# Performance work log

Hardware: AMD Instinct MI355X
Metric: run time of the kernel (lower is better)

Reference implementation:

```python
import jax, jax.numpy as jnp
import numpy as np
import itertools

R_MAX = 0.4
POWER = 0
B, N_ATOMS, K_OPS = 16, 256, 16

# 27 periodic image shifts, same order as itertools.product([0,1,-1], repeat=3)
SHIFTS = jnp.asarray(list(itertools.product([0, 1, -1], repeat=3)), dtype=jnp.float32)  # [27,3]


def _pair_sq_sum(f, r):
    """sum over neighbor pairs (dist<=r) of elementwise (frac_dst-frac_src)**2.

    Equivalent to torch get_neighbors (cdist over 27 shifted copies, radius
    mask, gather) followed by (vec*vec).sum(dim=0), without materializing
    the variable-length edge list. f: [N,3] -> out: [3]."""
    n = f.shape[0]
    # shift-major replication: f_ex[s*n + i] = f[i] + SHIFTS[s], matching
    # torch.cat([frac]*27) + shifts.repeat_interleave(n)
    f_ex = (f[None, :, :] + SHIFTS[:, None, :]).reshape(27 * n, 3)
    d = f_ex[None, :, :] - f[:, None, :]          # [N, 27N, 3] = dst - src
    dist2 = jnp.sum(d * d, axis=-1)               # [N, 27N]
    mask = (jnp.sqrt(dist2) <= r).astype(f.dtype)
    return jnp.einsum('ij,ijc->c', mask, d * d)   # [3]


def setup_inputs() -> dict:
    key = jax.random.key(0)
    k1, k2 = jax.random.split(key)
    fracs = jax.random.uniform(k1, (B * N_ATOMS, 3), dtype=jnp.float32)
    natms = jnp.full((B,), N_ATOMS, dtype=jnp.int32)
    oprss = jax.random.normal(k2, (B * K_OPS, 3, 3), dtype=jnp.float32)
    noprs = jnp.full((B,), K_OPS, dtype=jnp.int32)
    return {"fracs": fracs, "natms": natms, "oprss": oprss, "noprs": noprs}


def reference(fracs, natms, oprss, noprs):
    b = natms.shape[0]
    n = fracs.shape[0] // b          # uniform atoms per structure (static)
    k = oprss.shape[0] // noprs.shape[0]  # uniform operators per structure
    fr = fracs.reshape(b, n, 3)
    ops = oprss.reshape(b, k, 3, 3)
    r = R_MAX / (n ** POWER)

    def per_struct(loss, xs):
        f, opset = xs                        # [N,3], [K,3,3]
        out0 = _pair_sq_sum(f, r)            # identical for every opr

        def per_op(opr):
            f1 = (f @ opr.T) % 1.0
            return jnp.linalg.norm(_pair_sq_sum(f1, r) - out0)

        diffs = jax.vmap(per_op)(opset)      # [K]
        return loss + diffs.sum() / (k * b), None

    loss, _ = jax.lax.scan(per_struct, jnp.float32(0.0), (fr, ops))
    return loss
```

## Files before the change

### kernel.cpp

```cpp
#include <hip/hip_runtime.h>
#include <math.h>


#define NATOMS 256
#define KOPS   16
#define NB     16
#define TPB    17
#define NTASK  (NB * TPB)
#define NBLK   (NTASK * 2)

__device__ __forceinline__ float wrap01(float x) {
    float m = fmodf(x, 1.0f);
    if (m < 0.0f) m += 1.0f;
    return m;
}

__global__ __launch_bounds__(256) void pair_kernel(
    const float* __restrict__ fracs,
    const float* __restrict__ oprss,
    float* __restrict__ sums)
{
    const int blk  = blockIdx.x;
    const int task = blk >> 1;
    const int q    = blk & 1;
    const int b    = task / TPB;
    const int tt   = task - b * TPB;

    const int tid = threadIdx.x;
    const int h   = tid >> 7;
    const int i   = tid & 127;

    const float* f = fracs + (size_t)b * NATOMS * 3;

    __shared__ float4 sfE[256];
    __shared__ float4 sfO[256];

    {
        float fx = f[tid*3+0], fy = f[tid*3+1], fz = f[tid*3+2];
        if (tt > 0) {
            const float* op = oprss + (size_t)(b * KOPS + tt - 1) * 9;
            float gx = wrap01(fx*op[0] + fy*op[1] + fz*op[2]);
            float gy = wrap01(fx*op[3] + fy*op[4] + fz*op[5]);
            float gz = wrap01(fx*op[6] + fy*op[7] + fz*op[8]);
            fx = gx; fy = gy; fz = gz;
        }
        float4 v4 = make_float4(fx, fy, fz, 0.0f);
        if (tid & 1) sfO[tid >> 1] = v4; else sfE[tid >> 1] = v4;
        if (tid < 128) {
            if (tid & 1) sfO[128 + (tid >> 1)] = v4; else sfE[128 + (tid >> 1)] = v4;
        }
    }
    __syncthreads();

    const float4 fa = sfE[i];
    const float4 fb = sfO[i];

    float a2x = 0.f, a2y = 0.f, a2z = 0.f;
    float a1x = 0.f, a1y = 0.f, a1z = 0.f;

#define EVAL_INTO(FJ, S, AX, AY, AZ, SGN) do {                                 \
        float dx = (FJ).x - (S).x, dy = (FJ).y - (S).y, dz = (FJ).z - (S).z;   \
        float vx = dx - rintf(dx), vy = dy - rintf(dy), vz = dz - rintf(dz);   \
        float px = vx*vx, py = vy*vy, pz = vz*vz;                              \
        float d2 = px + py + pz;                                               \
        float m  = (d2 <= 0.16f) ? (SGN) : 0.0f;                               \
        AX = fmaf(px, m, AX); AY = fmaf(py, m, AY); AZ = fmaf(pz, m, AZ);      \
    } while (0)

    const int ebase = i + ((2 + (q*2 + h) * 32) >> 1);
    #pragma unroll
    for (int u = 0; u < 32; u += 2) {
        {
            const float4 fj = sfE[ebase + (u >> 1)];
            EVAL_INTO(fj, fa, a2x, a2y, a2z, 1.0f);
            EVAL_INTO(fj, fb, a2x, a2y, a2z, 1.0f);
        }
        {
            const float4 fj = sfO[ebase + (u >> 1)];
            EVAL_INTO(fj, fa, a2x, a2y, a2z, 1.0f);
            EVAL_INTO(fj, fb, a2x, a2y, a2z, 1.0f);
        }
    }

    if (q == 1 && h == 1) {
        EVAL_INTO(fb, fa, a2x, a2y, a2z, 1.0f);
        {   const float4 fj = sfE[i + 64];
            EVAL_INTO(fj, fa, a1x, a1y, a1z, -1.0f);
            EVAL_INTO(fj, fb, a1x, a1y, a1z, -1.0f);
        }
        {   const float4 fj = sfO[i + 64];
            EVAL_INTO(fj, fa, a1x, a1y, a1z, -1.0f);
            EVAL_INTO(fj, fb, a1x, a1y, a1z, -1.0f);
        }
    }
#undef EVAL_INTO

    float cx = fmaf(2.0f, a2x, a1x);
    float cy = fmaf(2.0f, a2y, a1y);
    float cz = fmaf(2.0f, a2z, a1z);

    for (int off = 32; off >= 1; off >>= 1) {
        cx += __shfl_xor(cx, off);
        cy += __shfl_xor(cy, off);
        cz += __shfl_xor(cz, off);
    }
    __shared__ float part[4][3];
    const int wave = tid >> 6;
    if ((tid & 63) == 0) { part[wave][0] = cx; part[wave][1] = cy; part[wave][2] = cz; }
    __syncthreads();
    if (tid == 0) {
        float* dst = sums + (size_t)blk * 3;
        dst[0] = part[0][0] + part[1][0] + part[2][0] + part[3][0];
        dst[1] = part[0][1] + part[1][1] + part[2][1] + part[3][1];
        dst[2] = part[0][2] + part[1][2] + part[2][2] + part[3][2];
    }
}

__global__ __launch_bounds__(256) void finish_kernel(
    const float* __restrict__ sums, float* __restrict__ out)
{
    const int t = threadIdx.x;
    const int b = t >> 4, k = t & 15;
    const float* s0p = sums + (size_t)((b * TPB + 0)     * 2) * 3;
    const float* skp = sums + (size_t)((b * TPB + 1 + k) * 2) * 3;
    float s0x = 0.f, s0y = 0.f, s0z = 0.f;
    float skx = 0.f, sky = 0.f, skz = 0.f;
    #pragma unroll
    for (int qq = 0; qq < 2; ++qq) {
        s0x += s0p[qq*3+0]; s0y += s0p[qq*3+1]; s0z += s0p[qq*3+2];
        skx += skp[qq*3+0]; sky += skp[qq*3+1]; skz += skp[qq*3+2];
    }
    float d0 = skx - s0x, d1 = sky - s0y, d2 = skz - s0z;
    float v = sqrtf(d0*d0 + d1*d1 + d2*d2);

    for (int off = 32; off >= 1; off >>= 1) v += __shfl_xor(v, off);
    __shared__ float part[4];
    if ((t & 63) == 0) part[t >> 6] = v;
    __syncthreads();
    if (t == 0) out[0] = (part[0] + part[1] + part[2] + part[3]) * (1.0f / 256.0f);
}

extern "C" void kernel_launch(void* const* d_in, const int* in_sizes, int n_in,
                              void* d_out, int out_size, void* d_ws, size_t ws_size,
                              hipStream_t stream) {
    const float* fracs = (const float*)d_in[0];
    const float* oprss = (const float*)d_in[2];
    float* out  = (float*)d_out;
    float* sums = (float*)d_ws;

    pair_kernel<<<NBLK, 256, 0, stream>>>(fracs, oprss, sums);
    finish_kernel<<<1, 256, 0, stream>>>(sums, out);
}
```

Measured before the change: 14.82 us.

## Fuse pair sums and final reduction into one kernel with atomic counters

Replaces the two-kernel scheme with one launch of 256 blocks of 1024 threads, one block per (structure, operator). Each block computes both the identity and the operator-transformed pair sums, takes the norm of their difference, and reduces globally through atomic adds plus self-resetting atomicDec counters, so the last block writes the output. This removes the second kernel launch and its dependency gap. In exchange, the identity sum is recomputed once per operator, nearly doubling the pair arithmetic. Correctness depends on the workspace starting at zero and on the atomics being ordered correctly without explicit fences.

```diff
diff --git a/kernel.cpp b/kernel.cpp
--- a/kernel.cpp
+++ b/kernel.cpp
@@ -5,9 +5,6 @@
 #define NATOMS 256
 #define KOPS   16
 #define NB     16
-#define TPB    17
-#define NTASK  (NB * TPB)
-#define NBLK   (NTASK * 2)
 
 __device__ __forceinline__ float wrap01(float x) {
     float m = fmodf(x, 1.0f);
@@ -15,48 +12,49 @@
     return m;
 }
 
-__global__ __launch_bounds__(256) void pair_kernel(
+__global__ __launch_bounds__(1024) void sgo_kernel(
     const float* __restrict__ fracs,
     const float* __restrict__ oprss,
-    float* __restrict__ sums)
+    float* __restrict__ ws,
+    float* __restrict__ out)
 {
-    const int blk  = blockIdx.x;
-    const int task = blk >> 1;
-    const int q    = blk & 1;
-    const int b    = task / TPB;
-    const int tt   = task - b * TPB;
-
+    const int blk = blockIdx.x;
+    const int b   = blk >> 4;
+    const int k   = blk & 15;
     const int tid = threadIdx.x;
-    const int h   = tid >> 7;
     const int i   = tid & 127;
+    const int c   = tid >> 7;
 
     const float* f = fracs + (size_t)b * NATOMS * 3;
 
-    __shared__ float4 sfE[256];
-    __shared__ float4 sfO[256];
+    __shared__ float4 idE[192], idO[192], opE[192], opO[192];
 
-    {
-        float fx = f[tid*3+0], fy = f[tid*3+1], fz = f[tid*3+2];
-        if (tt > 0) {
-            const float* op = oprss + (size_t)(b * KOPS + tt - 1) * 9;
+    if (tid < 512) {
+        const int atom = tid & 255;
+        float fx = f[atom*3+0], fy = f[atom*3+1], fz = f[atom*3+2];
+        if (tid >= 256) {
+            const float* op = oprss + (size_t)(b * KOPS + k) * 9;
             float gx = wrap01(fx*op[0] + fy*op[1] + fz*op[2]);
             float gy = wrap01(fx*op[3] + fy*op[4] + fz*op[5]);
             float gz = wrap01(fx*op[6] + fy*op[7] + fz*op[8]);
             fx = gx; fy = gy; fz = gz;
         }
         float4 v4 = make_float4(fx, fy, fz, 0.0f);
-        if (tid & 1) sfO[tid >> 1] = v4; else sfE[tid >> 1] = v4;
-        if (tid < 128) {
-            if (tid & 1) sfO[128 + (tid >> 1)] = v4; else sfE[128 + (tid >> 1)] = v4;
+        float4* arrE = (tid < 256) ? idE : opE;
+        float4* arrO = (tid < 256) ? idO : opO;
+        const int slot = atom >> 1;
+        if (atom & 1) arrO[slot] = v4; else arrE[slot] = v4;
+        if (atom < 128) {
+            if (atom & 1) arrO[128 + slot] = v4; else arrE[128 + slot] = v4;
         }
     }
     __syncthreads();
 
-    const float4 fa = sfE[i];
-    const float4 fb = sfO[i];
+    const float4 ia = idE[i], ib = idO[i];
+    const float4 oa = opE[i], ob = opO[i];
 
-    float a2x = 0.f, a2y = 0.f, a2z = 0.f;
-    float a1x = 0.f, a1y = 0.f, a1z = 0.f;
+    float i2x=0.f,i2y=0.f,i2z=0.f, i1x=0.f,i1y=0.f,i1z=0.f;
+    float o2x=0.f,o2y=0.f,o2z=0.f, o1x=0.f,o1y=0.f,o1z=0.f;
 
 #define EVAL_INTO(FJ, S, AX, AY, AZ, SGN) do {                                 \
         float dx = (FJ).x - (S).x, dy = (FJ).y - (S).y, dz = (FJ).z - (S).z;   \
@@ -67,77 +65,91 @@
         AX = fmaf(px, m, AX); AY = fmaf(py, m, AY); AZ = fmaf(pz, m, AZ);      \
     } while (0)
 
-    const int ebase = i + ((2 + (q*2 + h) * 32) >> 1);
+    const int eb = i + 1 + 8 * c;
     #pragma unroll
-    for (int u = 0; u < 32; u += 2) {
-        {
-            const float4 fj = sfE[ebase + (u >> 1)];
-            EVAL_INTO(fj, fa, a2x, a2y, a2z, 1.0f);
-            EVAL_INTO(fj, fb, a2x, a2y, a2z, 1.0f);
+    for (int u = 0; u < 8; ++u) {
+        {   const float4 fj = idE[eb + u];
+            EVAL_INTO(fj, ia, i2x, i2y, i2z, 1.0f);
+            EVAL_INTO(fj, ib, i2x, i2y, i2z, 1.0f);
         }
-        {
-            const float4 fj = sfO[ebase + (u >> 1)];
-            EVAL_INTO(fj, fa, a2x, a2y, a2z, 1.0f);
-            EVAL_INTO(fj, fb, a2x, a2y, a2z, 1.0f);
+        {   const float4 fj = opE[eb + u];
+            EVAL_INTO(fj, oa, o2x, o2y, o2z, 1.0f);
+            EVAL_INTO(fj, ob, o2x, o2y, o2z, 1.0f);
+        }
+        {   const float4 fj = idO[eb + u];
+            EVAL_INTO(fj, ia, i2x, i2y, i2z, 1.0f);
+            EVAL_INTO(fj, ib, i2x, i2y, i2z, 1.0f);
+        }
+        {   const float4 fj = opO[eb + u];
+            EVAL_INTO(fj, oa, o2x, o2y, o2z, 1.0f);
+            EVAL_INTO(fj, ob, o2x, o2y, o2z, 1.0f);
         }
     }
 
-    if (q == 1 && h == 1) {
-        EVAL_INTO(fb, fa, a2x, a2y, a2z, 1.0f);
-        {   const float4 fj = sfE[i + 64];
-            EVAL_INTO(fj, fa, a1x, a1y, a1z, -1.0f);
-            EVAL_INTO(fj, fb, a1x, a1y, a1z, -1.0f);
+    if (c == 7) {
+        EVAL_INTO(ib, ia, i2x, i2y, i2z, 1.0f);
+        EVAL_INTO(ob, oa, o2x, o2y, o2z, 1.0f);
+        {   const float4 fj = idE[i + 64];
+            EVAL_INTO(fj, ia, i1x, i1y, i1z, -1.0f);
+            EVAL_INTO(fj, ib, i1x, i1y, i1z, -1.0f);
         }
-        {   const float4 fj = sfO[i + 64];
-            EVAL_INTO(fj, fa, a1x, a1y, a1z, -1.0f);
-            EVAL_INTO(fj, fb, a1x, a1y, a1z, -1.0f);
+        {   const float4 fj = opE[i + 64];
+            EVAL_INTO(fj, oa, o1x, o1y, o1z, -1.0f);
+            EVAL_INTO(fj, ob, o1x, o1y, o1z, -1.0f);
+        }
+        {   const float4 fj = idO[i + 64];
+            EVAL_INTO(fj, ia, i1x, i1y, i1z, -1.0f);
+            EVAL_INTO(fj, ib, i1x, i1y, i1z, -1.0f);
+        }
+        {   const float4 fj = opO[i + 64];
+            EVAL_INTO(fj, oa, o1x, o1y, o1z, -1.0f);
+            EVAL_INTO(fj, ob, o1x, o1y, o1z, -1.0f);
         }
     }
 #undef EVAL_INTO
 
-    float cx = fmaf(2.0f, a2x, a1x);
-    float cy = fmaf(2.0f, a2y, a1y);
-    float cz = fmaf(2.0f, a2z, a1z);
+    float dxr = fmaf(2.0f, o2x, o1x) - fmaf(2.0f, i2x, i1x);
+    float dyr = fmaf(2.0f, o2y, o1y) - fmaf(2.0f, i2y, i1y);
+    float dzr = fmaf(2.0f, o2z, o1z) - fmaf(2.0f, i2z, i1z);
 
     for (int off = 32; off >= 1; off >>= 1) {
-        cx += __shfl_xor(cx, off);
-        cy += __shfl_xor(cy, off);
-        cz += __shfl_xor(cz, off);
+        dxr += __shfl_xor(dxr, off);
+        dyr += __shfl_xor(dyr, off);
+        dzr += __shfl_xor(dzr, off);
     }
-    __shared__ float part[4][3];
+    __shared__ float part[16][3];
     const int wave = tid >> 6;
-    if ((tid & 63) == 0) { part[wave][0] = cx; part[wave][1] = cy; part[wave][2] = cz; }
+    if ((tid & 63) == 0) { part[wave][0] = dxr; part[wave][1] = dyr; part[wave][2] = dzr; }
     __syncthreads();
+
     if (tid == 0) {
-        float* dst = sums + (size_t)blk * 3;
-        dst[0] = part[0][0] + part[1][0] + part[2][0] + part[3][0];
-        dst[1] = part[0][1] + part[1][1] + part[2][1] + part[3][1];
-        dst[2] = part[0][2] + part[1][2] + part[2][2] + part[3][2];
+        float sx = 0.f, sy = 0.f, sz = 0.f;
+        #pragma unroll
+        for (int w = 0; w < 16; ++w) {
+            sx += part[w][0]; sy += part[w][1]; sz += part[w][2];
+        }
+        float v = sqrtf(sx*sx + sy*sy + sz*sz) * (1.0f / 256.0f);
+
+        float*        partial = ws + (size_t)b * 64;
+        unsigned int* ctrb    = (unsigned int*)(ws + 1024 + b * 64);
+        float*        gacc    = ws + 2048;
+        unsigned int* gctr    = (unsigned int*)(ws + 2064);
+
+        float old = atomicAdd(partial, v);
+        asm volatile("" : : "v"(old) : "memory");
+        unsigned int o = atomicDec(ctrb, 15u);
+        if (o == 1u) {
+            float s = atomicExch(partial, 0.0f);
+            asm volatile("" : : "v"(s) : "memory");
+            float g = atomicAdd(gacc, s);
+            asm volatile("" : : "v"(g) : "memory");
+            unsigned int o2 = atomicDec(gctr, 15u);
+            if (o2 == 1u) {
+                float total = atomicExch(gacc, 0.0f);
+                out[0] = total;
+            }
+        }
     }
-}
-
-__global__ __launch_bounds__(256) void finish_kernel(
-    const float* __restrict__ sums, float* __restrict__ out)
-{
-    const int t = threadIdx.x;
-    const int b = t >> 4, k = t & 15;
-    const float* s0p = sums + (size_t)((b * TPB + 0)     * 2) * 3;
-    const float* skp = sums + (size_t)((b * TPB + 1 + k) * 2) * 3;
-    float s0x = 0.f, s0y = 0.f, s0z = 0.f;
-    float skx = 0.f, sky = 0.f, skz = 0.f;
-    #pragma unroll
-    for (int qq = 0; qq < 2; ++qq) {
-        s0x += s0p[qq*3+0]; s0y += s0p[qq*3+1]; s0z += s0p[qq*3+2];
-        skx += skp[qq*3+0]; sky += skp[qq*3+1]; skz += skp[qq*3+2];
-    }
-    float d0 = skx - s0x, d1 = sky - s0y, d2 = skz - s0z;
-    float v = sqrtf(d0*d0 + d1*d1 + d2*d2);
-
-    for (int off = 32; off >= 1; off >>= 1) v += __shfl_xor(v, off);
-    __shared__ float part[4];
-    if ((t & 63) == 0) part[t >> 6] = v;
-    __syncthreads();
-    if (t == 0) out[0] = (part[0] + part[1] + part[2] + part[3]) * (1.0f / 256.0f);
 }
 
 extern "C" void kernel_launch(void* const* d_in, const int* in_sizes, int n_in,
@@ -145,9 +157,8 @@
                               hipStream_t stream) {
     const float* fracs = (const float*)d_in[0];
     const float* oprss = (const float*)d_in[2];
-    float* out  = (float*)d_out;
-    float* sums = (float*)d_ws;
+    float* out = (float*)d_out;
+    float* ws  = (float*)d_ws;
 
-    pair_kernel<<<NBLK, 256, 0, stream>>>(fracs, oprss, sums);
-    finish_kernel<<<1, 256, 0, stream>>>(sums, out);
+    sgo_kernel<<<NB * KOPS, 1024, 0, stream>>>(fracs, oprss, ws, out);
 }
```

After: 17.27 us. 16.6% more time.
